# Optimization experiments

Hardware: AMD Instinct MI355X
Metric: run time of the kernel (lower is better)

Reference implementation:

```python
import jax, jax.numpy as jnp
import numpy as np
import math

B, S, D, H, NF = 2, 2048, 1024, 16, 4
DH = D // H


def setup_inputs() -> dict:
    key = jax.random.key(0)
    ks = jax.random.split(key, 8)
    scale = 0.01 / math.sqrt(D)  # rough attenuated-kaiming scale for projections
    return {
        "x": jax.random.normal(ks[0], (B, S, D), dtype=jnp.float32),
        "weights": jax.random.uniform(ks[1], (1, NF), dtype=jnp.float32),
        "Wq": jax.random.normal(ks[2], (D, D), dtype=jnp.float32) * scale,
        "bq": jnp.zeros((D,), dtype=jnp.float32),
        "Wk": jax.random.normal(ks[3], (D, D), dtype=jnp.float32) * scale,
        "bk": jnp.zeros((D,), dtype=jnp.float32),
        "Wv": jax.random.normal(ks[4], (D, D), dtype=jnp.float32) * scale,
        "bv": jnp.zeros((D,), dtype=jnp.float32),
        "Wout": jax.random.normal(ks[5], (NF, D, D), dtype=jnp.float32) / math.sqrt(D),
        "bout": jnp.zeros((NF, D), dtype=jnp.float32),
    }


def reference(x, weights, Wq, bq, Wk, bk, Wv, bv, Wout, bout):
    # projections (torch Linear: x @ W.T + b)
    q = x @ Wq.T + bq  # [B,S,D]
    k = x @ Wk.T + bk
    v = x @ Wv.T + bv
    # split heads -> [B,H,S,DH]
    split = lambda t: t.reshape(B, S, H, DH).transpose(0, 2, 1, 3)
    q, k, v = split(q), split(k), split(v)
    # scores with causal additive mask of -10000 (as in get_attention_mask)
    scores = jnp.einsum("bhqd,bhkd->bhqk", q, k) / math.sqrt(DH)
    i = jnp.arange(S)
    causal = (i[None, :] <= i[:, None])  # [S,S] True where allowed
    mask = (1.0 - causal.astype(scores.dtype)) * -10000.0
    attn = jax.nn.softmax(scores + mask, axis=-1)
    # dropout is disabled (p=0.0)
    out = jnp.einsum("bhqk,bhkd->bhqd", attn, v)  # [B,H,S,DH]
    out = out.transpose(0, 2, 1, 3).reshape(B, S, D)
    # WeightedFunctions: per-function Linear(d,d) combined by weights[0]
    w0 = weights[0]  # [NF]
    Weff = jnp.einsum("f,fod->od", w0, Wout)  # [D,D]
    beff = w0 @ bout  # [D]
    return out @ Weff.T + beff
```

## Files before the change

### kernel.cpp

```cpp
#include <hip/hip_runtime.h>

typedef unsigned short u16;
typedef __bf16 bf16_t;
typedef bf16_t bf16x8 __attribute__((ext_vector_type(8)));
typedef bf16_t bf16x4 __attribute__((ext_vector_type(4)));
typedef float f32x4 __attribute__((ext_vector_type(4)));
typedef u16 u16x8 __attribute__((ext_vector_type(8)));
typedef u16 u16x4 __attribute__((ext_vector_type(4)));

#define DEV __device__ __forceinline__

DEV u16 f2bf(float f) {
  unsigned u = __float_as_uint(f);
  u += 0x7FFFu + ((u >> 16) & 1u);
  return (u16)(u >> 16);
}

DEV void async_ld16(const void* g, void* lds_wave_uniform) {
  __builtin_amdgcn_global_load_lds(
      (const __attribute__((address_space(1))) void*)g,
      (__attribute__((address_space(3))) void*)lds_wave_uniform, 16, 0, 0);
}

DEV int KF(int r) { return (r & 3) ^ ((r >> 2) & 1); }

__global__ __launch_bounds__(256) void prep_kernel(
    const float* __restrict__ x, const float* __restrict__ Wq,
    const float* __restrict__ Wk, const float* __restrict__ Wv,
    const float* __restrict__ w4, const float* __restrict__ Wout,
    const float* __restrict__ bout, u16* __restrict__ xbf,
    u16* __restrict__ wqkv, u16* __restrict__ Weff, float* __restrict__ beff) {
  constexpr int NX = 1048576;
  constexpr int NW = 262144;
  const int stride = gridDim.x * 256;
  for (int id = blockIdx.x * 256 + threadIdx.x; id < NX + 3 * NW + NW;
       id += stride) {
    if (id < NX) {
      const float4 v = ((const float4*)x)[id];
      u16x4 o;
      o[0] = f2bf(v.x); o[1] = f2bf(v.y); o[2] = f2bf(v.z); o[3] = f2bf(v.w);
      ((u16x4*)xbf)[id] = o;
    } else if (id < NX + 3 * NW) {
      const int wi = id - NX;
      const int which = wi >> 18, j = wi & (NW - 1);
      const float* src = which == 0 ? Wq : (which == 1 ? Wk : Wv);
      const float4 v = ((const float4*)src)[j];
      u16x4 o;
      o[0] = f2bf(v.x); o[1] = f2bf(v.y); o[2] = f2bf(v.z); o[3] = f2bf(v.w);
      ((u16x4*)wqkv)[wi] = o;
    } else {
      const int i = id - NX - 3 * NW;
      const float w0 = w4[0], w1 = w4[1], w2 = w4[2], w3 = w4[3];
      const float4* W = (const float4*)Wout;
      const float4 a = W[i], b1 = W[NW + i], b2 = W[2 * NW + i],
                   b3 = W[3 * NW + i];
      u16x4 o;
      o[0] = f2bf(w0 * a.x + w1 * b1.x + w2 * b2.x + w3 * b3.x);
      o[1] = f2bf(w0 * a.y + w1 * b1.y + w2 * b2.y + w3 * b3.y);
      o[2] = f2bf(w0 * a.z + w1 * b1.z + w2 * b2.z + w3 * b3.z);
      o[3] = f2bf(w0 * a.w + w1 * b1.w + w2 * b2.w + w3 * b3.w);
      ((u16x4*)Weff)[i] = o;
      if (i < 256) {
        const float4* B4 = (const float4*)bout;
        const float4 ba = B4[i], c1 = B4[256 + i], c2 = B4[512 + i],
                     c3 = B4[768 + i];
        float4 ob;
        ob.x = w0 * ba.x + w1 * c1.x + w2 * c2.x + w3 * c3.x;
        ob.y = w0 * ba.y + w1 * c1.y + w2 * c2.y + w3 * c3.y;
        ob.z = w0 * ba.z + w1 * c1.z + w2 * c2.z + w3 * c3.z;
        ob.w = w0 * ba.w + w1 * c1.w + w2 * c2.w + w3 * c3.w;
        ((float4*)beff)[i] = ob;
      }
    }
  }
}

#define GEMM_PIPELINE_LOOP(A_, B_, m0_, n0_, K_)                               \
  int rA[2], oA[2], dstc[2];                                                   \
  _Pragma("unroll") for (int j = 0; j < 2; ++j) {                              \
    const int c = (j * 4 + w) * 64 + lane;                                     \
    rA[j] = c >> 2;                                                            \
    oA[j] = ((c & 3) ^ KF(rA[j])) * 8;                                         \
    dstc[j] = (j * 4 + w) * 512;                                               \
  }                                                                            \
  auto stage = [&](int buf, int kt) {                                          \
    _Pragma("unroll") for (int j = 0; j < 2; ++j) {                            \
      async_ld16(A_ + (m0_ + rA[j]) * K_ + kt + oA[j],                         \
                 &LDS[buf * 4096 + dstc[j]]);                                  \
      async_ld16(B_ + (n0_ + rA[j]) * K_ + kt + oA[j],                         \
                 &LDS[12288 + buf * 4096 + dstc[j]]);                          \
    }                                                                          \
  };                                                                           \
  f32x4 acc[4][4] = {};                                                        \
  stage(0, 0);                                                                 \
  stage(1, 32);                                                                \
  const int nt = K_ / 32;                                                      \
  int cur = 0, stg = 2;                                                        \
  for (int t = 0; t < nt; ++t) {                                               \
    if (t == nt - 1)                                                           \
      asm volatile("s_waitcnt vmcnt(0)\ns_barrier" ::: "memory");              \
    else                                                                       \
      asm volatile("s_waitcnt vmcnt(4)\ns_barrier" ::: "memory");              \
    __builtin_amdgcn_sched_barrier(0);                                         \
    if (t + 2 < nt) stage(stg, (t + 2) * 32);                                  \
    bf16x8 af[4], bfr[4];                                                      \
    _Pragma("unroll") for (int i = 0; i < 4; ++i) {                            \
      const int ra = wr * 64 + i * 16 + l15;                                   \
      const int rb = wc * 64 + i * 16 + l15;                                   \
      af[i] = *(const bf16x8*)&LDS[cur * 4096 + ra * 32 + ((l4 ^ KF(ra)) * 8)];\
      bfr[i] = *(const bf16x8*)&LDS[12288 + cur * 4096 + rb * 32 +             \
                                    ((l4 ^ KF(rb)) * 8)];                      \
    }                                                                          \
    __builtin_amdgcn_s_setprio(1);                                             \
    _Pragma("unroll") for (int i = 0; i < 4; ++i)                              \
        _Pragma("unroll") for (int j = 0; j < 4; ++j)                          \
            acc[i][j] = __builtin_amdgcn_mfma_f32_16x16x32_bf16(               \
                af[i], bfr[j], acc[i][j], 0, 0, 0);                            \
    __builtin_amdgcn_s_setprio(0);                                             \
    cur = cur == 2 ? 0 : cur + 1;                                              \
    stg = stg == 2 ? 0 : stg + 1;                                              \
  }

__global__ __launch_bounds__(256) void gemm_bt_kernel(
    const u16* __restrict__ A, const u16* __restrict__ Bw,
    const float* __restrict__ bias, float* __restrict__ C, int M, int N, int K) {
  __shared__ u16 LDS[24576];
  const int tid = threadIdx.x;
  const int w = tid >> 6, lane = tid & 63;
  const int l15 = lane & 15, l4 = lane >> 4;
  const int wr = w >> 1, wc = w & 1;
  const long m0 = (long)blockIdx.x * 128, n0 = (long)blockIdx.y * 128;

  GEMM_PIPELINE_LOOP(A, Bw, m0, n0, K)

#pragma unroll
  for (int i = 0; i < 4; ++i) {
    const long row0 = m0 + wr * 64 + i * 16 + l4 * 4;
#pragma unroll
    for (int j = 0; j < 4; ++j) {
      const long col = n0 + wc * 64 + j * 16 + l15;
      const float bb = bias[col];
#pragma unroll
      for (int r = 0; r < 4; ++r)
        C[(row0 + r) * N + col] = acc[i][j][r] + bb;
    }
  }
}

__global__ __launch_bounds__(512) void gemm_qkv_kernel(
    const u16* __restrict__ A, const u16* __restrict__ Bw,
    const float* __restrict__ bq, const float* __restrict__ bk,
    const float* __restrict__ bv, u16* __restrict__ qo, u16* __restrict__ ko,
    u16* __restrict__ vt) {
  constexpr int K = 1024;
  __shared__ u16 LDS[65536];
  const int tid = threadIdx.x;
  const int w = tid >> 6, lane = tid & 63;
  const int l15 = lane & 15, l4 = lane >> 4;
  const int wr = w >> 2, wc = w & 3;
  const long m0 = (long)blockIdx.y * 256, n0 = (long)blockIdx.x * 256;
  const int seg = blockIdx.x >> 2;
  const float* bias = seg == 0 ? bq : (seg == 1 ? bk : bv);
  const float scale = seg == 0 ? 0.18033688011112042f : 1.0f;

  const int sr0 = tid >> 3;
  const int soff = ((tid & 7) ^ ((tid >> 3) & 7)) * 8;
  auto stage_half = [&](int k, int h) {
    const int slot = k & 1;
    const int base =
        (h < 2 ? 0 : 32768) + slot * 16384 + (h & 1) * 8192;
    const long row0 = (h < 2 ? m0 : n0) + (h & 1) * 128;
    const u16* M = (h < 2) ? A : Bw;
    const int kt = k * 64;
    async_ld16(M + (row0 + sr0) * K + kt + soff, &LDS[base + w * 512]);
    async_ld16(M + (row0 + 64 + sr0) * K + kt + soff,
               &LDS[base + 4096 + w * 512]);
  };

  f32x4 acc[8][4] = {};
#pragma unroll
  for (int h = 0; h < 4; ++h) stage_half(0, h);

  for (int t = 0; t < 16; ++t) {
    asm volatile("s_waitcnt vmcnt(0)\ns_barrier" ::: "memory");
    const int slot = t & 1;
    const int abase = slot * 16384;
    const int bbase = 32768 + slot * 16384;
    const bool st = (t + 1) < 16;
    bf16x8 bfr[4][2];
#pragma unroll
    for (int j = 0; j < 4; ++j) {
      const int rb = wc * 64 + j * 16 + l15;
#pragma unroll
      for (int ks = 0; ks < 2; ++ks)
        bfr[j][ks] = *(const bf16x8*)&LDS[bbase + rb * 64 +
                                          (((ks * 4 + l4) ^ (rb & 7)) * 8)];
    }
#pragma unroll
    for (int ph = 0; ph < 4; ++ph) {
      if (st) stage_half(t + 1, ph);
      const int ra0 = wr * 128 + (2 * ph) * 16 + l15;
      const int ra1 = wr * 128 + (2 * ph + 1) * 16 + l15;
      bf16x8 af0[2], af1[2];
#pragma unroll
      for (int ks = 0; ks < 2; ++ks) {
        af0[ks] = *(const bf16x8*)&LDS[abase + ra0 * 64 +
                                       (((ks * 4 + l4) ^ (ra0 & 7)) * 8)];
        af1[ks] = *(const bf16x8*)&LDS[abase + ra1 * 64 +
                                       (((ks * 4 + l4) ^ (ra1 & 7)) * 8)];
      }
      __builtin_amdgcn_s_setprio(1);
#pragma unroll
      for (int j = 0; j < 4; ++j) {
        acc[2 * ph][j] = __builtin_amdgcn_mfma_f32_16x16x32_bf16(
            af0[0], bfr[j][0], acc[2 * ph][j], 0, 0, 0);
        acc[2 * ph][j] = __builtin_amdgcn_mfma_f32_16x16x32_bf16(
            af0[1], bfr[j][1], acc[2 * ph][j], 0, 0, 0);
        acc[2 * ph + 1][j] = __builtin_amdgcn_mfma_f32_16x16x32_bf16(
            af1[0], bfr[j][0], acc[2 * ph + 1][j], 0, 0, 0);
        acc[2 * ph + 1][j] = __builtin_amdgcn_mfma_f32_16x16x32_bf16(
            af1[1], bfr[j][1], acc[2 * ph + 1][j], 0, 0, 0);
      }
      __builtin_amdgcn_s_setprio(0);
    }
  }

  __syncthreads();
  const long ccol0 = n0 - (long)seg * 1024;
  if (seg < 2) {
    u16* outp = seg == 0 ? qo : ko;
#pragma unroll
    for (int h = 0; h < 2; ++h) {
      if ((wc >> 1) == h) {
#pragma unroll
        for (int i = 0; i < 8; ++i)
#pragma unroll
          for (int j = 0; j < 4; ++j) {
            const int colb = (wc & 1) * 64 + j * 16 + l15;
            const float bb = bias[ccol0 + h * 128 + colb];
#pragma unroll
            for (int r = 0; r < 4; ++r) {
              const int row = wr * 128 + i * 16 + l4 * 4 + r;
              LDS[row * 128 + (colb ^ ((row & 15) << 3))] =
                  f2bf((acc[i][j][r] + bb) * scale);
            }
          }
      }
      __syncthreads();
#pragma unroll
      for (int p = 0; p < 8; ++p) {
        const int cid = p * 512 + tid;
        const int row = cid >> 4, c = cid & 15;
        const u16x8 vch =
            *(const u16x8*)&LDS[row * 128 + ((c ^ (row & 15)) * 8)];
        *(u16x8*)&outp[(m0 + row) * 1024 + ccol0 + h * 128 + c * 8] = vch;
      }
      __syncthreads();
    }
  } else {
    const int b = (int)(m0 >> 11);
    const int s0 = (int)(m0 & 2047);
#pragma unroll
    for (int h = 0; h < 2; ++h) {
      if ((wc >> 1) == h) {
#pragma unroll
        for (int i = 0; i < 8; ++i)
#pragma unroll
          for (int j = 0; j < 4; ++j) {
            const int colb = (wc & 1) * 64 + j * 16 + l15;
            const float bb = bias[ccol0 + h * 128 + colb];
#pragma unroll
            for (int r = 0; r < 4; ++r) {
              const int row = wr * 128 + i * 16 + l4 * 4 + r;
              LDS[colb * 256 + (row ^ ((colb & 15) << 3))] =
                  f2bf(acc[i][j][r] + bb);
            }
          }
      }
      __syncthreads();
#pragma unroll
      for (int p = 0; p < 8; ++p) {
        const int cid = p * 512 + tid;
        const int c = cid >> 5, r0 = (cid & 31) * 8;
        const u16x8 vch = *(const u16x8*)&LDS[c * 256 + (r0 ^ ((c & 15) << 3))];
        const int gcol = (int)ccol0 + h * 128 + c;
        const int hh = gcol >> 6, d = gcol & 63;
        *(u16x8*)&vt[(size_t)((b * 16 + hh) * 64 + d) * 2048 + s0 + r0] = vch;
      }
      __syncthreads();
    }
  }
}

__global__ __launch_bounds__(512) void flash_kernel(
    const u16* __restrict__ Q, const u16* __restrict__ Kg,
    const u16* __restrict__ Vt, u16* __restrict__ O,
    u16* __restrict__ accP, float* __restrict__ mP, float* __restrict__ lP) {
  constexpr int S = 2048, D = 1024, DH = 64;
  __shared__ u16 Ks[3][4096];
  __shared__ u16 Vs[3][4096];
  __shared__ u16 Ps[8][2048];
  const int tid = threadIdx.x;
  const int w = tid >> 6, lane = tid & 63;
  const int l15 = lane & 15, l4 = lane >> 4;
  const int bh = blockIdx.x, b = bh >> 4, h = bh & 15;
  const int xb = blockIdx.y;
  const int p = xb >> 1, seg = xb & 1;
  const int p1len = seg ? 0 : 4 * p + 4;
  const int kvoff = seg ? (14 - 4 * p) : 0;
  const int TA = seg ? (7 - p) : p;
  const int TB = 7 - p;
  const int qbA_keep = TA * 256 + w * 32;

  const u16* Kbh = Kg + (size_t)b * S * D + h * DH;
  const u16* Vbh = Vt + (size_t)bh * DH * S;

  const int srow = tid >> 3;
  const int scol = ((tid & 7) ^ (srow & 7)) * 8;
  const int sw = l15 & 7;

  bf16x8 qf[2][2], qfB[2][2];
#pragma unroll
  for (int c = 0; c < 2; ++c) {
    const u16* qp =
        Q + (size_t)(b * S + qbA_keep + c * 16 + l15) * D + h * DH + l4 * 8;
    qf[c][0] = *(const bf16x8*)qp;
    qf[c][1] = *(const bf16x8*)(qp + 32);
    qfB[c][0] = qf[c][0];
    qfB[c][1] = qf[c][1];
  }
  if (!seg) {
    const int qbB = TB * 256 + w * 32;
#pragma unroll
    for (int c = 0; c < 2; ++c) {
      const u16* qp =
          Q + (size_t)(b * S + qbB + c * 16 + l15) * D + h * DH + l4 * 8;
      qfB[c][0] = *(const bf16x8*)qp;
      qfB[c][1] = *(const bf16x8*)(qp + 32);
    }
  }

  f32x4 acc_o[2][4] = {};
  float m_run[2] = {-3e38f, -3e38f};
  float l_run[2] = {0.f, 0.f};

  int qb = qbA_keep;
  int qt64w = TA * 4 + (w >> 1);

  auto kv_of = [&](int j) { return (j < p1len) ? j : (j - p1len + kvoff); };
  auto stage = [&](int kv, int buf) {
    async_ld16(Kbh + (size_t)(kv * 64 + srow) * D + scol, &Ks[buf][w * 512]);
    async_ld16(Vbh + (size_t)srow * S + kv * 64 + scol, &Vs[buf][w * 512]);
  };

  stage(kv_of(0), 0);
  stage(kv_of(1), 1);

  constexpr int NST = 18;
  for (int j = 0; j < NST; ++j) {
    if (j == NST - 1)
      asm volatile("s_waitcnt vmcnt(0)\ns_barrier" ::: "memory");
    else
      asm volatile("s_waitcnt vmcnt(2)\ns_barrier" ::: "memory");
    __builtin_amdgcn_sched_barrier(0);
    if (j + 2 < NST) stage(kv_of(j + 2), (j + 2) % 3);

    if (seg == 0 && j == p1len) {
      float lt[2], lq[2][4];
#pragma unroll
      for (int c = 0; c < 2; ++c) {
        float t = l_run[c];
        t += __shfl_xor(t, 16);
        t += __shfl_xor(t, 32);
        lt[c] = t;
#pragma unroll
        for (int r = 0; r < 4; ++r) lq[c][r] = __shfl(lt[c], l4 * 4 + r, 64);
      }
#pragma unroll
      for (int c = 0; c < 2; ++c)
#pragma unroll
        for (int db = 0; db < 4; ++db)
#pragma unroll
          for (int r = 0; r < 4; ++r) {
            const int row = c * 16 + l4 * 4 + r;
            const int col = db * 16 + l15;
            Ps[w][row * 64 + (col ^ ((row & 7) << 3))] =
                f2bf(acc_o[c][db][r] / lq[c][r]);
          }
      asm volatile("s_waitcnt lgkmcnt(0)" ::: "memory");
#pragma unroll
      for (int j4 = 0; j4 < 4; ++j4) {
        const int cid = j4 * 64 + lane;
        const int row = cid >> 3, c8 = cid & 7;
        const u16x8 vch =
            *(const u16x8*)&Ps[w][row * 64 + ((c8 ^ (row & 7)) * 8)];
        *(u16x8*)&O[(size_t)(b * S + qbA_keep + row) * D + h * DH + c8 * 8] =
            vch;
      }
#pragma unroll
      for (int c = 0; c < 2; ++c) {
        qf[c][0] = qfB[c][0];
        qf[c][1] = qfB[c][1];
        m_run[c] = -3e38f;
        l_run[c] = 0.f;
#pragma unroll
        for (int db = 0; db < 4; ++db) acc_o[c][db] = f32x4{0.f, 0.f, 0.f, 0.f};
      }
      qb = TB * 256 + w * 32;
      qt64w = TB * 4 + (w >> 1);
    }

    const int it = kv_of(j);
    const int buf = j % 3;
    if (it <= qt64w) {
      f32x4 accs[2][4] = {};
      __builtin_amdgcn_s_setprio(1);
#pragma unroll
      for (int cb = 0; cb < 4; ++cb) {
        const int row = cb * 16 + l15;
        const bf16x8 kf0 = *(const bf16x8*)&Ks[buf][row * 64 + ((l4 ^ sw) * 8)];
        const bf16x8 kf1 =
            *(const bf16x8*)&Ks[buf][row * 64 + (((l4 + 4) ^ sw) * 8)];
#pragma unroll
        for (int c = 0; c < 2; ++c) {
          accs[c][cb] = __builtin_amdgcn_mfma_f32_16x16x32_bf16(
              kf0, qf[c][0], accs[c][cb], 0, 0, 0);
          accs[c][cb] = __builtin_amdgcn_mfma_f32_16x16x32_bf16(
              kf1, qf[c][1], accs[c][cb], 0, 0, 0);
        }
      }
      __builtin_amdgcn_s_setprio(0);
      bf16x8 vf0[4], vf1[4];
#pragma unroll
      for (int db = 0; db < 4; ++db) {
        const int row = db * 16 + l15;
        vf0[db] = *(const bf16x8*)&Vs[buf][row * 64 + ((l4 ^ sw) * 8)];
        vf1[db] = *(const bf16x8*)&Vs[buf][row * 64 + (((l4 + 4) ^ sw) * 8)];
      }
      float mx[2] = {-3e38f, -3e38f};
      if (it == qt64w) {
#pragma unroll
        for (int c = 0; c < 2; ++c)
#pragma unroll
          for (int cb = 0; cb < 4; ++cb)
#pragma unroll
            for (int r = 0; r < 4; ++r) {
              float s_ = accs[c][cb][r];
              if (it * 64 + cb * 16 + l4 * 4 + r > qb + c * 16 + l15)
                s_ = -3e38f;
              accs[c][cb][r] = s_;
              mx[c] = fmaxf(mx[c], s_);
            }
      } else {
#pragma unroll
        for (int c = 0; c < 2; ++c)
#pragma unroll
          for (int cb = 0; cb < 4; ++cb)
#pragma unroll
            for (int r = 0; r < 4; ++r) mx[c] = fmaxf(mx[c], accs[c][cb][r]);
      }
      if (!__all(fmaxf(mx[0] - m_run[0], mx[1] - m_run[1]) <= 8.0f)) {
#pragma unroll
        for (int c = 0; c < 2; ++c) {
          float m = mx[c];
          m = fmaxf(m, __shfl_xor(m, 16));
          m = fmaxf(m, __shfl_xor(m, 32));
          const float mn = fmaxf(m_run[c], m);
          const float corr = __builtin_amdgcn_exp2f(m_run[c] - mn);
          m_run[c] = mn;
          float cq[4];
#pragma unroll
          for (int r = 0; r < 4; ++r) cq[r] = __shfl(corr, l4 * 4 + r, 64);
#pragma unroll
          for (int db = 0; db < 4; ++db)
#pragma unroll
            for (int r = 0; r < 4; ++r) acc_o[c][db][r] *= cq[r];
          l_run[c] *= corr;
        }
      }
#pragma unroll
      for (int c = 0; c < 2; ++c) {
        float rs = 0.f;
#pragma unroll
        for (int cb = 0; cb < 4; ++cb)
#pragma unroll
          for (int r = 0; r < 4; ++r) {
            const float pv = __builtin_amdgcn_exp2f(accs[c][cb][r] - m_run[c]);
            accs[c][cb][r] = pv;
            rs += pv;
          }
        l_run[c] += rs;
      }
#pragma unroll
      for (int c = 0; c < 2; ++c)
#pragma unroll
        for (int cb = 0; cb < 4; ++cb) {
          bf16x4 pk = {(bf16_t)accs[c][cb][0], (bf16_t)accs[c][cb][1],
                       (bf16_t)accs[c][cb][2], (bf16_t)accs[c][cb][3]};
          const int chunk = (2 * cb + (l4 >> 1)) ^ sw;
          *(bf16x4*)&Ps[w][(c * 16 + l15) * 64 + chunk * 8 + (l4 & 1) * 4] = pk;
        }
      asm volatile("s_waitcnt lgkmcnt(0)" ::: "memory");
      bf16x8 pa[2][2];
#pragma unroll
      for (int c = 0; c < 2; ++c)
#pragma unroll
        for (int mf = 0; mf < 2; ++mf) {
          const int chunk = (mf * 4 + l4) ^ sw;
          pa[c][mf] =
              *(const bf16x8*)&Ps[w][(c * 16 + l15) * 64 + chunk * 8];
        }
      __builtin_amdgcn_s_setprio(1);
#pragma unroll
      for (int db = 0; db < 4; ++db) {
#pragma unroll
        for (int c = 0; c < 2; ++c) {
          acc_o[c][db] = __builtin_amdgcn_mfma_f32_16x16x32_bf16(
              pa[c][0], vf0[db], acc_o[c][db], 0, 0, 0);
          acc_o[c][db] = __builtin_amdgcn_mfma_f32_16x16x32_bf16(
              pa[c][1], vf1[db], acc_o[c][db], 0, 0, 0);
        }
      }
      __builtin_amdgcn_s_setprio(0);
    }
  }

  float lt[2];
#pragma unroll
  for (int c = 0; c < 2; ++c) {
    float t = l_run[c];
    t += __shfl_xor(t, 16);
    t += __shfl_xor(t, 32);
    lt[c] = t;
  }
#pragma unroll
  for (int c = 0; c < 2; ++c)
#pragma unroll
    for (int db = 0; db < 4; ++db)
#pragma unroll
      for (int r = 0; r < 4; ++r) {
        const int row = c * 16 + l4 * 4 + r;
        const int col = db * 16 + l15;
        Ps[w][row * 64 + (col ^ ((row & 7) << 3))] = f2bf(acc_o[c][db][r]);
      }
  asm volatile("s_waitcnt lgkmcnt(0)" ::: "memory");
  const size_t base =
      (size_t)seg * 32768 + (size_t)bh * 1024 + (TB * 256 + w * 32 - 1024);
#pragma unroll
  for (int j4 = 0; j4 < 4; ++j4) {
    const int cid = j4 * 64 + lane;
    const int row = cid >> 3, c8 = cid & 7;
    const u16x8 vch = *(const u16x8*)&Ps[w][row * 64 + ((c8 ^ (row & 7)) * 8)];
    *(u16x8*)&accP[(base + row) * 64 + c8 * 8] = vch;
  }
  if (l4 == 0) {
#pragma unroll
    for (int c = 0; c < 2; ++c) {
      mP[base + c * 16 + l15] = m_run[c];
      lP[base + c * 16 + l15] = lt[c];
    }
  }
}

__global__ __launch_bounds__(256) void combine_kernel(
    const u16* __restrict__ accP, const float* __restrict__ mP,
    const float* __restrict__ lP, u16* __restrict__ O) {
  const int id = blockIdx.x * 256 + threadIdx.x;
  const int row = id >> 3;
  const int c0 = (id & 7) * 8;
  const float m0 = mP[row], m1 = mP[32768 + row];
  const float l0 = lP[row], l1 = lP[32768 + row];
  const float M = fmaxf(m0, m1);
  const float e0 = __builtin_amdgcn_exp2f(m0 - M);
  const float e1 = __builtin_amdgcn_exp2f(m1 - M);
  const float inv = 1.f / (l0 * e0 + l1 * e1);
  const bf16_t* aP = (const bf16_t*)accP;
  const bf16x8 a0 = *(const bf16x8*)&aP[(size_t)row * 64 + c0];
  const bf16x8 a1 = *(const bf16x8*)&aP[(size_t)(32768 + row) * 64 + c0];
  const int bh = row >> 10, s = 1024 + (row & 1023);
  const int b = bh >> 4, h = bh & 15;
  bf16_t* out = (bf16_t*)O + (size_t)(b * 2048 + s) * 1024 + h * 64 + c0;
  bf16x8 o;
#pragma unroll
  for (int j = 0; j < 8; ++j)
    o[j] = (bf16_t)(((float)a0[j] * e0 + (float)a1[j] * e1) * inv);
  *(bf16x8*)out = o;
}

extern "C" void kernel_launch(void* const* d_in, const int* in_sizes, int n_in,
                              void* d_out, int out_size, void* d_ws, size_t ws_size,
                              hipStream_t stream) {
  (void)in_sizes; (void)n_in; (void)out_size;
  const float* x   = (const float*)d_in[0];
  const float* wts = (const float*)d_in[1];
  const float* Wq  = (const float*)d_in[2];
  const float* bq  = (const float*)d_in[3];
  const float* Wk  = (const float*)d_in[4];
  const float* bk  = (const float*)d_in[5];
  const float* Wv  = (const float*)d_in[6];
  const float* bv  = (const float*)d_in[7];
  const float* Wo  = (const float*)d_in[8];
  const float* bo  = (const float*)d_in[9];
  float* out = (float*)d_out;

  if (ws_size < 58724352) return;

  char* ws = (char*)d_ws;
  u16* xbf  = (u16*)(ws + 0);
  u16* qbf  = (u16*)(ws + 8388608);
  u16* kbf  = (u16*)(ws + 16777216);
  u16* vt   = (u16*)(ws + 33554432);
  u16* attn = (u16*)(ws + 41943040);
  u16* wqkv = (u16*)(ws + 50331648);
  u16* wob  = (u16*)(ws + 56623104);
  float* beff = (float*)(ws + 58720256);

  u16* accP = xbf;
  float* mP = (float*)(ws + 50331648);
  float* lP = mP + 65536;

  prep_kernel<<<2048, 256, 0, stream>>>(x, Wq, Wk, Wv, wts, Wo, bo,
                                        xbf, wqkv, wob, beff);
  gemm_qkv_kernel<<<dim3(12, 16), 512, 0, stream>>>(xbf, wqkv, bq, bk, bv,
                                                    qbf, kbf, vt);
  flash_kernel<<<dim3(32, 8), 512, 0, stream>>>(qbf, kbf, vt, attn,
                                                accP, mP, lP);
  combine_kernel<<<1024, 256, 0, stream>>>(accP, mP, lP, attn);
  gemm_bt_kernel<<<dim3(32, 8), 256, 0, stream>>>(
      attn, wob, beff, out, 4096, 1024, 1024);
}
```

Before: 103.3 us.

## Restructure output GEMM to BK=64 double-buffer with interleaved staging

```diff
diff --git a/kernel.cpp b/kernel.cpp
--- a/kernel.cpp
+++ b/kernel.cpp
@@ -21,8 +21,6 @@
       (const __attribute__((address_space(1))) void*)g,
       (__attribute__((address_space(3))) void*)lds_wave_uniform, 16, 0, 0);
 }
-
-DEV int KF(int r) { return (r & 3) ^ ((r >> 2) & 1); }
 
 __global__ __launch_bounds__(256) void prep_kernel(
     const float* __restrict__ x, const float* __restrict__ Wq,
@@ -75,63 +73,71 @@
   }
 }
 
-#define GEMM_PIPELINE_LOOP(A_, B_, m0_, n0_, K_)                               \
-  int rA[2], oA[2], dstc[2];                                                   \
-  _Pragma("unroll") for (int j = 0; j < 2; ++j) {                              \
-    const int c = (j * 4 + w) * 64 + lane;                                     \
-    rA[j] = c >> 2;                                                            \
-    oA[j] = ((c & 3) ^ KF(rA[j])) * 8;                                         \
-    dstc[j] = (j * 4 + w) * 512;                                               \
-  }                                                                            \
-  auto stage = [&](int buf, int kt) {                                          \
-    _Pragma("unroll") for (int j = 0; j < 2; ++j) {                            \
-      async_ld16(A_ + (m0_ + rA[j]) * K_ + kt + oA[j],                         \
-                 &LDS[buf * 4096 + dstc[j]]);                                  \
-      async_ld16(B_ + (n0_ + rA[j]) * K_ + kt + oA[j],                         \
-                 &LDS[12288 + buf * 4096 + dstc[j]]);                          \
-    }                                                                          \
-  };                                                                           \
-  f32x4 acc[4][4] = {};                                                        \
-  stage(0, 0);                                                                 \
-  stage(1, 32);                                                                \
-  const int nt = K_ / 32;                                                      \
-  int cur = 0, stg = 2;                                                        \
-  for (int t = 0; t < nt; ++t) {                                               \
-    if (t == nt - 1)                                                           \
-      asm volatile("s_waitcnt vmcnt(0)\ns_barrier" ::: "memory");              \
-    else                                                                       \
-      asm volatile("s_waitcnt vmcnt(4)\ns_barrier" ::: "memory");              \
-    __builtin_amdgcn_sched_barrier(0);                                         \
-    if (t + 2 < nt) stage(stg, (t + 2) * 32);                                  \
-    bf16x8 af[4], bfr[4];                                                      \
-    _Pragma("unroll") for (int i = 0; i < 4; ++i) {                            \
-      const int ra = wr * 64 + i * 16 + l15;                                   \
-      const int rb = wc * 64 + i * 16 + l15;                                   \
-      af[i] = *(const bf16x8*)&LDS[cur * 4096 + ra * 32 + ((l4 ^ KF(ra)) * 8)];\
-      bfr[i] = *(const bf16x8*)&LDS[12288 + cur * 4096 + rb * 32 +             \
-                                    ((l4 ^ KF(rb)) * 8)];                      \
-    }                                                                          \
-    __builtin_amdgcn_s_setprio(1);                                             \
-    _Pragma("unroll") for (int i = 0; i < 4; ++i)                              \
-        _Pragma("unroll") for (int j = 0; j < 4; ++j)                          \
-            acc[i][j] = __builtin_amdgcn_mfma_f32_16x16x32_bf16(               \
-                af[i], bfr[j], acc[i][j], 0, 0, 0);                            \
-    __builtin_amdgcn_s_setprio(0);                                             \
-    cur = cur == 2 ? 0 : cur + 1;                                              \
-    stg = stg == 2 ? 0 : stg + 1;                                              \
-  }
-
 __global__ __launch_bounds__(256) void gemm_bt_kernel(
     const u16* __restrict__ A, const u16* __restrict__ Bw,
     const float* __restrict__ bias, float* __restrict__ C, int M, int N, int K) {
-  __shared__ u16 LDS[24576];
+  __shared__ u16 LDS[32768];
   const int tid = threadIdx.x;
   const int w = tid >> 6, lane = tid & 63;
   const int l15 = lane & 15, l4 = lane >> 4;
   const int wr = w >> 1, wc = w & 1;
   const long m0 = (long)blockIdx.x * 128, n0 = (long)blockIdx.y * 128;
 
-  GEMM_PIPELINE_LOOP(A, Bw, m0, n0, K)
+  int rS[4], oS[4], dS[4];
+#pragma unroll
+  for (int j = 0; j < 4; ++j) {
+    const int c = (j * 4 + w) * 64 + lane;
+    rS[j] = c >> 3;
+    oS[j] = ((c & 7) ^ (rS[j] & 7)) * 8;
+    dS[j] = (j * 4 + w) * 512;
+  }
+  auto stage_pt = [&](int k, int j) {
+    const int slot = k & 1;
+    const int kt = k * 64;
+    async_ld16(A + (m0 + rS[j]) * K + kt + oS[j], &LDS[slot * 8192 + dS[j]]);
+    async_ld16(Bw + (n0 + rS[j]) * K + kt + oS[j],
+               &LDS[16384 + slot * 8192 + dS[j]]);
+  };
+
+  f32x4 acc[4][4] = {};
+#pragma unroll
+  for (int j = 0; j < 4; ++j) stage_pt(0, j);
+
+  const int nt = K / 64;
+  for (int t = 0; t < nt; ++t) {
+    asm volatile("s_waitcnt vmcnt(0)\ns_barrier" ::: "memory");
+    const int abase = (t & 1) * 8192;
+    const int bbase = 16384 + (t & 1) * 8192;
+    const bool st = (t + 1) < nt;
+    bf16x8 bfr[4][2];
+#pragma unroll
+    for (int j = 0; j < 4; ++j) {
+      const int rb = wc * 64 + j * 16 + l15;
+#pragma unroll
+      for (int ks = 0; ks < 2; ++ks)
+        bfr[j][ks] = *(const bf16x8*)&LDS[bbase + rb * 64 +
+                                          (((ks * 4 + l4) ^ (rb & 7)) * 8)];
+    }
+#pragma unroll
+    for (int ph = 0; ph < 4; ++ph) {
+      if (st) stage_pt(t + 1, ph);
+      const int ra = wr * 64 + ph * 16 + l15;
+      bf16x8 af[2];
+#pragma unroll
+      for (int ks = 0; ks < 2; ++ks)
+        af[ks] = *(const bf16x8*)&LDS[abase + ra * 64 +
+                                      (((ks * 4 + l4) ^ (ra & 7)) * 8)];
+      __builtin_amdgcn_s_setprio(1);
+#pragma unroll
+      for (int j = 0; j < 4; ++j) {
+        acc[ph][j] = __builtin_amdgcn_mfma_f32_16x16x32_bf16(
+            af[0], bfr[j][0], acc[ph][j], 0, 0, 0);
+        acc[ph][j] = __builtin_amdgcn_mfma_f32_16x16x32_bf16(
+            af[1], bfr[j][1], acc[ph][j], 0, 0, 0);
+      }
+      __builtin_amdgcn_s_setprio(0);
+    }
+  }
 
 #pragma unroll
   for (int i = 0; i < 4; ++i) {
```

Result: no change. 104.6 us (+1.3%).
